# Kernel optimization log

Measured on AMD Instinct MI355X. Metric: run time of the kernel, lower is better.

## Reference

```python
import jax, jax.numpy as jnp
import numpy as np

B, L, IDIM = 1, 1024, 2048
H, DK, DV, K = 16, 128, 128, 4
KEY_DIM = H * DK          # 2048
VAL_DIM = H * DV          # 2048
CONV_DIM = 2 * KEY_DIM + VAL_DIM  # 6144
EPS = 1e-6


def setup_inputs() -> dict:
    key = jax.random.key(0)
    ks = jax.random.split(key, 8)
    s = 0.02
    x = jax.random.normal(ks[0], (B, L, IDIM), jnp.float32)
    Wqkv = jax.random.normal(ks[1], (IDIM, CONV_DIM), jnp.float32) * s
    Wz = jax.random.normal(ks[2], (IDIM, VAL_DIM), jnp.float32) * s
    Wb = jax.random.normal(ks[3], (IDIM, H), jnp.float32) * s
    Wa = jax.random.normal(ks[4], (IDIM, H), jnp.float32) * s
    conv_w = jax.random.normal(ks[5], (CONV_DIM, 1, K), jnp.float32) * 0.2  # depthwise [O,I/g=1,K]
    A_log = jnp.log(jax.random.uniform(ks[6], (H,), jnp.float32, 0.1, 16.0))
    dt_bias = jnp.ones((H,), jnp.float32)
    norm_w = jnp.ones((DV,), jnp.float32)
    Wout = jax.random.normal(ks[7], (VAL_DIM, IDIM), jnp.float32) * s
    return dict(x=x, Wqkv=Wqkv, Wz=Wz, Wb=Wb, Wa=Wa, conv_w=conv_w,
                A_log=A_log, dt_bias=dt_bias, norm_w=norm_w, Wout=Wout)


def _l2norm(t):
    return t * jax.lax.rsqrt(jnp.sum(t * t, axis=-1, keepdims=True) + EPS)


def reference(x, Wqkv, Wz, Wb, Wa, conv_w, A_log, dt_bias, norm_w, Wout):
    b, l, _ = x.shape
    # fused QKV projection + causal depthwise conv + SiLU
    qkv = jnp.einsum('bld,dc->blc', x, Wqkv)                 # [B,L,CONV_DIM]
    qkv = jnp.transpose(qkv, (0, 2, 1))                      # [B,C,L]
    qkv = jax.lax.conv_general_dilated(
        qkv, conv_w, window_strides=(1,), padding=[(K - 1, 0)],
        dimension_numbers=('NCL', 'OIL', 'NCL'), feature_group_count=CONV_DIM)
    qkv = jax.nn.silu(jnp.transpose(qkv, (0, 2, 1)))         # [B,L,C]
    q, k, v = jnp.split(qkv, [KEY_DIM, 2 * KEY_DIM], axis=-1)

    z = jnp.einsum('bld,dv->blv', x, Wz)                     # [B,L,VAL_DIM]
    beta = jax.nn.sigmoid(jnp.einsum('bld,dh->blh', x, Wb))  # [B,L,H]
    A = -jnp.exp(A_log)                                      # [H]
    dt = jax.nn.softplus(jnp.einsum('bld,dh->blh', x, Wa) + dt_bias)
    g = dt * A                                               # [B,L,H] (negative)

    q = _l2norm(q.reshape(b, l, H, DK))
    k = _l2norm(k.reshape(b, l, H, DK))
    v = v.reshape(b, l, H, DV)
    scale = DK ** -0.5

    # time-major for scan: [L,B,H,...]
    qs = jnp.transpose(q, (1, 0, 2, 3)) * scale
    ks_ = jnp.transpose(k, (1, 0, 2, 3))
    vs = jnp.transpose(v, (1, 0, 2, 3))
    bs = jnp.transpose(beta, (1, 0, 2))
    gs = jnp.transpose(g, (1, 0, 2))

    M0 = jnp.zeros((b, H, DK, DV), jnp.float32)

    def step(M, inp):
        q_t, k_t, v_t, b_t, g_t = inp
        M = M * jnp.exp(g_t)[..., None, None]                    # decay
        Mk = jnp.einsum('bhd,bhdv->bhv', k_t, M)                 # readout of old mem
        M = M + jnp.einsum('bhd,bhv->bhdv', k_t, (v_t - Mk) * b_t[..., None])
        o_t = jnp.einsum('bhd,bhdv->bhv', q_t, M)
        return M, o_t

    _, out = jax.lax.scan(step, M0, (qs, ks_, vs, bs, gs))   # out: [L,B,H,DV]
    out = jnp.transpose(out, (1, 0, 2, 3))                   # [B,L,H,DV]

    # RMSNormGated: rms_norm(o) * weight * silu(z)
    zg = z.reshape(b, l, H, DV)
    rms = jax.lax.rsqrt(jnp.mean(out * out, axis=-1, keepdims=True) + EPS)
    out = (out * rms) * norm_w * jax.nn.silu(zg)

    out = out.reshape(b, l, VAL_DIM)
    return jnp.einsum('blv,vd->bld', out, Wout)
```

## Files before the change

### kernel.cpp

```cpp
#include <hip/hip_runtime.h>

typedef short bf16x8 __attribute__((ext_vector_type(8)));
typedef float f32x4 __attribute__((ext_vector_type(4)));
typedef float f32x2 __attribute__((ext_vector_type(2)));
typedef unsigned short u16;
typedef u16 u16x4 __attribute__((ext_vector_type(4)));

#define L_SEQ 1024
#define IDIM_ 2048
#define H_ 16
#define DK_ 128
#define DV_ 128
#define KEYD 2048
#define VALD 2048
#define CONVD 6144
#define QZD 8320
#define GCOL 8192
#define CH 16
#define NCH (L_SEQ / CH)
#define SCH 64
#define NSC (L_SEQ / SCH)

__device__ __forceinline__ u16 f2bf(float f) {
  union { float f; unsigned u; } v; v.f = f;
  unsigned r = v.u + 0x7FFF + ((v.u >> 16) & 1);
  return (u16)(r >> 16);
}

__device__ __forceinline__ float red16(float x) {
  union U { float f; int i; } a, t;
  a.f = x;
  t.i = __builtin_amdgcn_update_dpp(0, a.i, 0xB1, 0xF, 0xF, true); a.f += t.f;
  t.i = __builtin_amdgcn_update_dpp(0, a.i, 0x4E, 0xF, 0xF, true); a.f += t.f;
  t.i = __builtin_amdgcn_update_dpp(0, a.i, 0x141, 0xF, 0xF, true); a.f += t.f;
  t.i = __builtin_amdgcn_update_dpp(0, a.i, 0x140, 0xF, 0xF, true); a.f += t.f;
  return a.f;
}

__device__ __forceinline__ void gl_lds16(const float* g, float* l) {
  __builtin_amdgcn_global_load_lds(
      (const __attribute__((address_space(1))) void*)g,
      (__attribute__((address_space(3))) void*)l, 16, 0, 0);
}
__device__ __forceinline__ void gl_lds4(const float* g, float* l) {
  __builtin_amdgcn_global_load_lds(
      (const __attribute__((address_space(1))) void*)g,
      (__attribute__((address_space(3))) void*)l, 4, 0, 0);
}

__global__ __launch_bounds__(256) void prepcast_kernel(const float* __restrict__ x,
                                                       const float* __restrict__ Wqkv,
                                                       const float* __restrict__ Wz,
                                                       const float* __restrict__ Wb,
                                                       const float* __restrict__ Wa,
                                                       const float* __restrict__ Wout,
                                                       u16* __restrict__ xb,
                                                       u16* __restrict__ WcatT,
                                                       u16* __restrict__ WoutT) {
  __shared__ float tile[32][33];
  const int bid = blockIdx.x;
  if (bid < 2048) {
    int i = (bid * 256 + threadIdx.x) * 4;
    f32x4 v = *(const f32x4*)&x[i];
    u16x4 o = { f2bf(v[0]), f2bf(v[1]), f2bf(v[2]), f2bf(v[3]) };
    *(u16x4*)&xb[i] = o;
    return;
  }
  if (bid >= 22592) {
    size_t off = (size_t)8224 * IDIM_ + (size_t)(bid - 22592) * 8192 + threadIdx.x * 32;
    u16x4 z = {0, 0, 0, 0};
#pragma unroll
    for (int j = 0; j < 8; ++j) *(u16x4*)&WcatT[off + j * 4] = z;
    return;
  }
  if (bid >= 22528) {
    int by = bid - 22528;
    int r = threadIdx.x >> 3, c8 = threadIdx.x & 7;
    int row = by * 32 + r;
#pragma unroll
    for (int cc = 0; cc < 2; ++cc) {
      int c = cc * 8 + c8;
      WcatT[(size_t)(GCOL + c) * IDIM_ + row]      = f2bf(Wb[(size_t)row * 16 + c]);
      WcatT[(size_t)(GCOL + 16 + c) * IDIM_ + row] = f2bf(Wa[(size_t)row * 16 + c]);
    }
    return;
  }
  const float* W; u16* WT; int R, C, bx, by;
  if (bid < 14336) {
    int t = bid - 2048;  bx = t % 192; by = t / 192;
    W = Wqkv; WT = WcatT; R = IDIM_; C = CONVD;
  } else if (bid < 18432) {
    int t = bid - 14336; bx = t & 63; by = t >> 6;
    W = Wz; WT = WcatT + (size_t)CONVD * IDIM_; R = IDIM_; C = VALD;
  } else {
    int t = bid - 18432; bx = t & 63; by = t >> 6;
    W = Wout; WT = WoutT; R = VALD; C = IDIM_;
  }
  int c0 = bx * 32, r0 = by * 32;
  int tx = threadIdx.x & 31, ty = threadIdx.x >> 5;
#pragma unroll
  for (int j = 0; j < 4; ++j)
    tile[ty + j * 8][tx] = W[(size_t)(r0 + ty + j * 8) * C + c0 + tx];
  __syncthreads();
#pragma unroll
  for (int j = 0; j < 4; ++j)
    WT[(size_t)(c0 + ty + j * 8) * R + r0 + tx] = f2bf(tile[tx][ty + j * 8]);
}

__global__ __launch_bounds__(256) void gemm_bt_kernel(const u16* __restrict__ A,
                                                      const u16* __restrict__ B,
                                                      float* __restrict__ C,
                                                      int M, int N, int K) {
  __shared__ short As[128 * 72];
  __shared__ short Bs[128 * 72];
  const int tid = threadIdx.x;
  const int lane = tid & 63, wave = tid >> 6;
  const int wm = wave >> 1, wn = wave & 1;
  const int m0 = blockIdx.y * 128, n0 = blockIdx.x * 128;
  const int l15 = lane & 15, lhi = lane >> 4;

  f32x4 acc[4][4] = {};

  for (int k0 = 0; k0 < K; k0 += 64) {
    __syncthreads();
#pragma unroll
    for (int i = 0; i < 4; ++i) {
      int chunk = tid + i * 256;
      int row = chunk >> 3;
      int kc = (chunk & 7) * 8;
      *(bf16x8*)&As[row * 72 + kc] =
          *(const bf16x8*)&A[(size_t)(m0 + row) * K + k0 + kc];
      *(bf16x8*)&Bs[row * 72 + kc] =
          *(const bf16x8*)&B[(size_t)(n0 + row) * K + k0 + kc];
    }
    __syncthreads();
#pragma unroll
    for (int kk = 0; kk < 64; kk += 32) {
      const int koff = kk + lhi * 8;
      bf16x8 a[4], b[4];
#pragma unroll
      for (int m = 0; m < 4; ++m)
        a[m] = *(const bf16x8*)&As[(wm * 64 + m * 16 + l15) * 72 + koff];
#pragma unroll
      for (int n = 0; n < 4; ++n)
        b[n] = *(const bf16x8*)&Bs[(wn * 64 + n * 16 + l15) * 72 + koff];
#pragma unroll
      for (int m = 0; m < 4; ++m)
#pragma unroll
        for (int n = 0; n < 4; ++n)
          acc[m][n] = __builtin_amdgcn_mfma_f32_16x16x32_bf16(a[m], b[n], acc[m][n], 0, 0, 0);
    }
  }
#pragma unroll
  for (int m = 0; m < 4; ++m)
#pragma unroll
    for (int n = 0; n < 4; ++n)
#pragma unroll
      for (int j = 0; j < 4; ++j) {
        int row = m0 + wm * 64 + m * 16 + lhi * 4 + j;
        int col = n0 + wn * 64 + n * 16 + l15;
        C[(size_t)row * N + col] = acc[m][n][j];
      }
}

__global__ __launch_bounds__(256) void gemm_bt64_kernel(const u16* __restrict__ A,
                                                        const u16* __restrict__ B,
                                                        float* __restrict__ C,
                                                        int M, int N, int K, int cxl) {
  __shared__ short As[64 * 72];
  __shared__ short Bs[128 * 72];
  const int tid = threadIdx.x;
  const int lane = tid & 63, wave = tid >> 6;
  const int wm = wave >> 1, wn = wave & 1;
  const int bid = blockIdx.x;
  const int xcd = bid & 7, bi = bid >> 3;
  const int bx = (xcd << cxl) + (bi & ((1 << cxl) - 1));
  const int by = bi >> cxl;
  const int m0 = by * 64, n0 = bx * 128;
  const int l15 = lane & 15, lhi = lane >> 4;

  f32x4 acc[2][4] = {};

  for (int k0 = 0; k0 < K; k0 += 64) {
    __syncthreads();
#pragma unroll
    for (int i = 0; i < 2; ++i) {
      int chunk = tid + i * 256;
      int row = chunk >> 3;
      int kc = (chunk & 7) * 8;
      *(bf16x8*)&As[row * 72 + kc] =
          *(const bf16x8*)&A[(size_t)(m0 + row) * K + k0 + kc];
    }
#pragma unroll
    for (int i = 0; i < 4; ++i) {
      int chunk = tid + i * 256;
      int row = chunk >> 3;
      int kc = (chunk & 7) * 8;
      *(bf16x8*)&Bs[row * 72 + kc] =
          *(const bf16x8*)&B[(size_t)(n0 + row) * K + k0 + kc];
    }
    __syncthreads();
#pragma unroll
    for (int kk = 0; kk < 64; kk += 32) {
      const int koff = kk + lhi * 8;
      bf16x8 a[2], b[4];
#pragma unroll
      for (int m = 0; m < 2; ++m)
        a[m] = *(const bf16x8*)&As[(wm * 32 + m * 16 + l15) * 72 + koff];
#pragma unroll
      for (int n = 0; n < 4; ++n)
        b[n] = *(const bf16x8*)&Bs[(wn * 64 + n * 16 + l15) * 72 + koff];
#pragma unroll
      for (int m = 0; m < 2; ++m)
#pragma unroll
        for (int n = 0; n < 4; ++n)
          acc[m][n] = __builtin_amdgcn_mfma_f32_16x16x32_bf16(a[m], b[n], acc[m][n], 0, 0, 0);
    }
  }
#pragma unroll
  for (int m = 0; m < 2; ++m)
#pragma unroll
    for (int n = 0; n < 4; ++n)
#pragma unroll
      for (int j = 0; j < 4; ++j) {
        int row = m0 + wm * 32 + m * 16 + lhi * 4 + j;
        int col = n0 + wn * 64 + n * 16 + l15;
        C[(size_t)row * N + col] = acc[m][n][j];
      }
}

__global__ __launch_bounds__(256) void gatelite_kernel(const float* __restrict__ qkvz,
                                                       const float* __restrict__ A_log,
                                                       const float* __restrict__ dt_bias,
                                                       float* __restrict__ btT,
                                                       float* __restrict__ egT,
                                                       float* __restrict__ gT) {
  int gid = blockIdx.x * 256 + threadIdx.x;
  int l = gid >> 4, h = gid & 15;
  const float* row = qkvz + (size_t)l * QZD + GCOL;
  float b = row[h], a = row[16 + h];
  btT[h * L_SEQ + l] = 1.f / (1.f + expf(-b));
  float dtv = a + dt_bias[h];
  dtv = (dtv > 20.f) ? dtv : log1pf(expf(dtv));
  float g = -expf(A_log[h]) * dtv;
  egT[h * L_SEQ + l] = expf(g);
  gT[h * L_SEQ + l] = g;
}

__global__ __launch_bounds__(256) void prep2_kernel(const float* __restrict__ qkvz,
                                                    const float* __restrict__ cw,
                                                    float* __restrict__ qn,
                                                    float* __restrict__ kn,
                                                    float* __restrict__ vT) {
  __shared__ float tile[32][33];
  const int bid = blockIdx.x;
  if (bid < 4096) {
    int wid = bid * 4 + (threadIdx.x >> 6);
    int lane = threadIdx.x & 63;
    int l = wid >> 4, h = wid & 15;
    const int cq = h * 128 + lane * 2;
    const int ck = KEYD + cq;
    const float* row0 = qkvz + (size_t)l * QZD;
    f32x4 wq0 = *(const f32x4*)&cw[cq * 4];
    f32x4 wq1 = *(const f32x4*)&cw[(cq + 1) * 4];
    f32x4 wk0 = *(const f32x4*)&cw[ck * 4];
    f32x4 wk1 = *(const f32x4*)&cw[(ck + 1) * 4];
    f32x2 xq = *(const f32x2*)&row0[cq];
    f32x2 xk = *(const f32x2*)&row0[ck];
    float q0 = xq[0] * wq0[3], q1 = xq[1] * wq1[3];
    float k0 = xk[0] * wk0[3], k1 = xk[1] * wk1[3];
    if (l >= 1) {
      f32x2 aq = *(const f32x2*)&row0[cq - QZD];
      f32x2 ak = *(const f32x2*)&row0[ck - QZD];
      q0 += aq[0] * wq0[2]; q1 += aq[1] * wq1[2];
      k0 += ak[0] * wk0[2]; k1 += ak[1] * wk1[2];
    }
    if (l >= 2) {
      f32x2 aq = *(const f32x2*)&row0[cq - 2 * QZD];
      f32x2 ak = *(const f32x2*)&row0[ck - 2 * QZD];
      q0 += aq[0] * wq0[1]; q1 += aq[1] * wq1[1];
      k0 += ak[0] * wk0[1]; k1 += ak[1] * wk1[1];
    }
    if (l >= 3) {
      f32x2 aq = *(const f32x2*)&row0[cq - 3 * QZD];
      f32x2 ak = *(const f32x2*)&row0[ck - 3 * QZD];
      q0 += aq[0] * wq0[0]; q1 += aq[1] * wq1[0];
      k0 += ak[0] * wk0[0]; k1 += ak[1] * wk1[0];
    }
    f32x2 qv = { q0 / (1.f + expf(-q0)), q1 / (1.f + expf(-q1)) };
    f32x2 kv = { k0 / (1.f + expf(-k0)), k1 / (1.f + expf(-k1)) };

    float ssq = qv[0] * qv[0] + qv[1] * qv[1];
    float ssk = kv[0] * kv[0] + kv[1] * kv[1];
#pragma unroll
    for (int s = 1; s < 64; s <<= 1) {
      ssq += __shfl_xor(ssq, s);
      ssk += __shfl_xor(ssk, s);
    }
    float scq = 0.08838834764831845f / sqrtf(ssq + 1e-6f);
    float sck = 1.f / sqrtf(ssk + 1e-6f);
    qv[0] *= scq; qv[1] *= scq;
    kv[0] *= sck; kv[1] *= sck;
    size_t base = ((size_t)h * L_SEQ + l) * 128 + lane * 2;
    *(f32x2*)&qn[base] = qv;
    *(f32x2*)&kn[base] = kv;
    return;
  }
  int t = bid - 4096;
  int c0 = (t & 63) * 32, l0 = (t >> 6) * 32;
  int tx = threadIdx.x & 31, ty = threadIdx.x >> 5;
  const int c = 2 * KEYD + c0 + tx;
  f32x4 w = *(const f32x4*)&cw[c * 4];
#pragma unroll
  for (int j = 0; j < 4; ++j) {
    int l = l0 + ty + j * 8;
    const float* p = qkvz + (size_t)l * QZD + c;
    float s = p[0] * w[3];
    if (l >= 1) s += p[-QZD] * w[2];
    if (l >= 2) s += p[-2 * QZD] * w[1];
    if (l >= 3) s += p[-3 * QZD] * w[0];
    tile[ty + j * 8][tx] = s / (1.f + expf(-s));
  }
  __syncthreads();
#pragma unroll
  for (int j = 0; j < 4; ++j)
    vT[(size_t)(c0 + ty + j * 8) * L_SEQ + l0 + tx] = tile[tx][ty + j * 8];
}

__global__ __launch_bounds__(256) void scan_kernel(const float* __restrict__ kn,
                                                   const float* __restrict__ vT,
                                                   const float* __restrict__ egT,
                                                   const float* __restrict__ btT,
                                                   float* __restrict__ Mb,
                                                   float* __restrict__ DbT) {
  __shared__ alignas(16) float ks[2][CH][128];
  __shared__ alignas(16) float vs[2][16][CH];
  __shared__ alignas(16) float ebc[2][2][CH];

  const int tid = threadIdx.x;
  const int wave = tid >> 6, lane = tid & 63;
  const int dk_sub = lane & 15;
  const int head = blockIdx.x & 15;
  const int dv0 = (blockIdx.x >> 4) * 16;
  const int col_local = tid >> 4;
  const int dv = dv0 + col_local;

  const float* kh = kn + (size_t)head * L_SEQ * 128;

  auto stage = [&](int chunk, int buf) {
    const int l0 = chunk * CH;
    const float* kg = kh + (size_t)l0 * 128;
#pragma unroll
    for (int i = 0; i < 2; ++i) {
      int seg = i * 4 + wave;
      int off = seg * 256 + lane * 4;
      gl_lds16(kg + off, &ks[buf][0][0] + seg * 256);
    }
    {
      int idx = wave * 64 + lane;
      gl_lds4(vT + (size_t)(head * 128 + dv0 + (idx >> 4)) * L_SEQ + l0 + (idx & 15),
              &vs[buf][0][0] + wave * 64);
    }
    if (wave == 0 && lane < 32) {
      const float* src = (lane < 16) ? (egT + head * L_SEQ + l0 + lane)
                                     : (btT + head * L_SEQ + l0 + (lane - 16));
      gl_lds4(src, &ebc[buf][0][0]);
    }
  };

  stage(0, 0);
  __syncthreads();

  f32x4 Mlo = {0.f, 0.f, 0.f, 0.f}, Mhi = {0.f, 0.f, 0.f, 0.f};
  const int dkb = dk_sub * 8;
  float* dcol = DbT + (size_t)(head * 128 + dv) * L_SEQ;

#pragma unroll 1
  for (int c = 0; c < NCH; ++c) {
    const int buf = c & 1;
    if (c + 1 < NCH) stage(c + 1, buf ^ 1);

    if ((c & 3) == 0) {
      int sc = c >> 2;
      float* mrow = Mb + (((size_t)sc * 16 + head) * 128 + dv) * 128 + dkb;
      *(f32x4*)mrow = Mlo;
      *(f32x4*)(mrow + 4) = Mhi;
    }

    f32x4 ev[4], bv[4], vv[4];
#pragma unroll
    for (int i = 0; i < 4; ++i) {
      ev[i] = *(const f32x4*)&ebc[buf][0][i * 4];
      bv[i] = *(const f32x4*)&ebc[buf][1][i * 4];
      vv[i] = *(const f32x4*)&vs[buf][col_local][i * 4];
    }
    f32x4 kr[4][2];
#pragma unroll
    for (int i = 0; i < 3; ++i) {
      kr[i][0] = *(const f32x4*)&ks[buf][i][dkb];
      kr[i][1] = *(const f32x4*)&ks[buf][i][dkb + 4];
    }

#pragma unroll
    for (int s = 0; s < CH; ++s) {
      if (s + 3 < CH) {
        kr[(s + 3) & 3][0] = *(const f32x4*)&ks[buf][s + 3][dkb];
        kr[(s + 3) & 3][1] = *(const f32x4*)&ks[buf][s + 3][dkb + 4];
      }
      const f32x4 k0 = kr[s & 3][0], k1 = kr[s & 3][1];
      const float e = ev[s >> 2][s & 3], b = bv[s >> 2][s & 3];
      const float v = vv[s >> 2][s & 3];

      float skm0 = k0[0] * Mlo[0], skm1 = k0[1] * Mlo[1];
      skm0 = fmaf(k0[2], Mlo[2], skm0); skm1 = fmaf(k0[3], Mlo[3], skm1);
      skm0 = fmaf(k1[0], Mhi[0], skm0); skm1 = fmaf(k1[1], Mhi[1], skm1);
      skm0 = fmaf(k1[2], Mhi[2], skm0); skm1 = fmaf(k1[3], Mhi[3], skm1);
      f32x4 emlo, emhi;
#pragma unroll
      for (int i = 0; i < 4; ++i) { emlo[i] = e * Mlo[i]; emhi[i] = e * Mhi[i]; }
      float skm = red16(skm0 + skm1);
      float dl = (v - e * skm) * b;
      if (dk_sub == 0) dcol[c * CH + s] = dl;
#pragma unroll
      for (int i = 0; i < 4; ++i) {
        Mlo[i] = fmaf(k0[i], dl, emlo[i]);
        Mhi[i] = fmaf(k1[i], dl, emhi[i]);
      }
    }
    __syncthreads();
  }
}

__global__ __launch_bounds__(256) void opass_kernel(const float* __restrict__ qn,
                                                    const float* __restrict__ kn,
                                                    const float* __restrict__ DbT,
                                                    const float* __restrict__ gT,
                                                    const float* __restrict__ Mb,
                                                    const float* __restrict__ qkvz,
                                                    const float* __restrict__ norm_w,
                                                    u16* __restrict__ gn) {
  __shared__ alignas(16) u16 qsb[64][136];
  __shared__ alignas(16) u16 bbuf[128][136];
  __shared__ alignas(16) u16 Asb[64][72];
  __shared__ float gsh[64], Gh[64];
  __shared__ float ssr[2][64];

  const int tid = threadIdx.x;
  const int lane = tid & 63, wave = tid >> 6;
  const int l15 = lane & 15, lhi = lane >> 4;
  const int h = blockIdx.x & 15, sc = blockIdx.x >> 4;
  const int l0 = sc * SCH;

  {
    int t = tid >> 2, c0 = (tid & 3) * 32;
    const float* qr = qn + ((size_t)h * L_SEQ + l0 + t) * 128 + c0;
    const float* kr = kn + ((size_t)h * L_SEQ + l0 + t) * 128 + c0;
#pragma unroll
    for (int j = 0; j < 8; ++j) {
      f32x4 vq = *(const f32x4*)&qr[j * 4];
      f32x4 vk = *(const f32x4*)&kr[j * 4];
      u16x4 oq = { f2bf(vq[0]), f2bf(vq[1]), f2bf(vq[2]), f2bf(vq[3]) };
      u16x4 ok = { f2bf(vk[0]), f2bf(vk[1]), f2bf(vk[2]), f2bf(vk[3]) };
      *(u16x4*)&qsb[t][c0 + j * 4] = oq;
      *(u16x4*)&bbuf[t][c0 + j * 4] = ok;
    }
  }
  if (tid < 64) gsh[tid] = gT[h * L_SEQ + l0 + tid];
  __syncthreads();
  if (tid < 64) {
    float a = 0.f;
    for (int u = 0; u <= tid; ++u) a += gsh[u];
    Gh[tid] = a;
  }
  __syncthreads();

  f32x4 acc1[2][2] = {};
  const int wm = wave >> 1, wn = wave & 1;
#pragma unroll
  for (int kk = 0; kk < 128; kk += 32) {
    const int koff = kk + lhi * 8;
    bf16x8 a[2], b[2];
#pragma unroll
    for (int m = 0; m < 2; ++m)
      a[m] = *(const bf16x8*)&qsb[wm * 32 + m * 16 + l15][koff];
#pragma unroll
    for (int n = 0; n < 2; ++n)
      b[n] = *(const bf16x8*)&bbuf[wn * 32 + n * 16 + l15][koff];
#pragma unroll
    for (int m = 0; m < 2; ++m)
#pragma unroll
      for (int n = 0; n < 2; ++n)
        acc1[m][n] = __builtin_amdgcn_mfma_f32_16x16x32_bf16(a[m], b[n], acc1[m][n], 0, 0, 0);
  }
#pragma unroll
  for (int m = 0; m < 2; ++m)
#pragma unroll
    for (int n = 0; n < 2; ++n)
#pragma unroll
      for (int j = 0; j < 4; ++j) {
        int t = wm * 32 + m * 16 + lhi * 4 + j;
        int s = wn * 32 + n * 16 + l15;
        float a = (s <= t) ? acc1[m][n][j] * expf(Gh[t] - Gh[s]) : 0.f;
        Asb[t][s] = f2bf(a);
      }
  __syncthreads();

  {
    int dv = tid >> 1, c0 = (tid & 1) * 64;
    const float* mr = Mb + (((size_t)sc * 16 + h) * 128 + dv) * 128 + c0;
#pragma unroll
    for (int j = 0; j < 16; ++j) {
      f32x4 v = *(const f32x4*)&mr[j * 4];
      u16x4 o = { f2bf(v[0]), f2bf(v[1]), f2bf(v[2]), f2bf(v[3]) };
      *(u16x4*)&bbuf[dv][c0 + j * 4] = o;
    }
  }
  __syncthreads();

  f32x4 acc[2][4] = {};
#pragma unroll
  for (int kk = 0; kk < 128; kk += 32) {
    const int koff = kk + lhi * 8;
    bf16x8 a[2], b[4];
#pragma unroll
    for (int m = 0; m < 2; ++m)
      a[m] = *(const bf16x8*)&qsb[wm * 32 + m * 16 + l15][koff];
#pragma unroll
    for (int n = 0; n < 4; ++n)
      b[n] = *(const bf16x8*)&bbuf[wn * 64 + n * 16 + l15][koff];
#pragma unroll
    for (int m = 0; m < 2; ++m)
#pragma unroll
      for (int n = 0; n < 4; ++n)
        acc[m][n] = __builtin_amdgcn_mfma_f32_16x16x32_bf16(a[m], b[n], acc[m][n], 0, 0, 0);
  }
#pragma unroll
  for (int m = 0; m < 2; ++m) {
#pragma unroll
    for (int j = 0; j < 4; ++j) {
      int t = wm * 32 + m * 16 + lhi * 4 + j;
      float sc1 = expf(Gh[t]);
#pragma unroll
      for (int n = 0; n < 4; ++n) acc[m][n][j] *= sc1;
    }
  }
  __syncthreads();

  {
    int dv = tid >> 1, c0 = (tid & 1) * 32;
    const float* dr = DbT + (size_t)(h * 128 + dv) * L_SEQ + l0 + c0;
#pragma unroll
    for (int j = 0; j < 8; ++j) {
      f32x4 v = *(const f32x4*)&dr[j * 4];
      u16x4 o = { f2bf(v[0]), f2bf(v[1]), f2bf(v[2]), f2bf(v[3]) };
      *(u16x4*)&bbuf[dv][c0 + j * 4] = o;
    }
  }
  __syncthreads();

#pragma unroll
  for (int kk = 0; kk < 64; kk += 32) {
    const int koff = kk + lhi * 8;
    bf16x8 a[2], b[4];
#pragma unroll
    for (int m = 0; m < 2; ++m)
      a[m] = *(const bf16x8*)&Asb[wm * 32 + m * 16 + l15][koff];
#pragma unroll
    for (int n = 0; n < 4; ++n)
      b[n] = *(const bf16x8*)&bbuf[wn * 64 + n * 16 + l15][koff];
#pragma unroll
    for (int m = 0; m < 2; ++m)
#pragma unroll
      for (int n = 0; n < 4; ++n)
        acc[m][n] = __builtin_amdgcn_mfma_f32_16x16x32_bf16(a[m], b[n], acc[m][n], 0, 0, 0);
  }

  float pr[2][4];
#pragma unroll
  for (int m = 0; m < 2; ++m)
#pragma unroll
    for (int j = 0; j < 4; ++j) {
      float p = 0.f;
#pragma unroll
      for (int n = 0; n < 4; ++n) p = fmaf(acc[m][n][j], acc[m][n][j], p);
      pr[m][j] = red16(p);
    }
  if (l15 == 0) {
#pragma unroll
    for (int m = 0; m < 2; ++m)
#pragma unroll
      for (int j = 0; j < 4; ++j)
        ssr[wn][wm * 32 + m * 16 + lhi * 4 + j] = pr[m][j];
  }
  __syncthreads();
#pragma unroll
  for (int m = 0; m < 2; ++m)
#pragma unroll
    for (int j = 0; j < 4; ++j) {
      int t = wm * 32 + m * 16 + lhi * 4 + j;
      float ss = ssr[0][t] + ssr[1][t];
      float r = 1.f / sqrtf(ss * (1.f / 128.f) + 1e-6f);
      const float* zp = qkvz + (size_t)(l0 + t) * QZD + CONVD + h * 128;
      u16* dst = gn + (size_t)(l0 + t) * VALD + h * 128;
#pragma unroll
      for (int n = 0; n < 4; ++n) {
        int dv = wn * 64 + n * 16 + l15;
        float z = zp[dv];
        float sil = z / (1.f + expf(-z));
        dst[dv] = f2bf(acc[m][n][j] * r * norm_w[dv] * sil);
      }
    }
}

extern "C" void kernel_launch(void* const* d_in, const int* in_sizes, int n_in,
                              void* d_out, int out_size, void* d_ws, size_t ws_size,
                              hipStream_t stream) {
  const float* x      = (const float*)d_in[0];
  const float* Wqkv   = (const float*)d_in[1];
  const float* Wz     = (const float*)d_in[2];
  const float* Wb     = (const float*)d_in[3];
  const float* Wa     = (const float*)d_in[4];
  const float* conv_w = (const float*)d_in[5];
  const float* A_log  = (const float*)d_in[6];
  const float* dt_bias= (const float*)d_in[7];
  const float* norm_w = (const float*)d_in[8];
  const float* Wout   = (const float*)d_in[9];
  float* out = (float*)d_out;

  char* ws = (char*)d_ws;
  size_t off = 0;
  auto alloc = [&](size_t bytes) {
    void* p = ws + off;
    off = (off + bytes + 255) & ~(size_t)255;
    return p;
  };
  u16* xb     = (u16*)alloc((size_t)L_SEQ * IDIM_ * 2);
  u16* WcatT  = (u16*)alloc((size_t)QZD * IDIM_ * 2);
  u16* WoutT  = (u16*)alloc((size_t)IDIM_ * VALD * 2);
  float* qkvz = (float*)alloc((size_t)L_SEQ * QZD * 4);
  float* qn   = (float*)alloc((size_t)H_ * L_SEQ * 128 * 4);
  float* kn   = (float*)alloc((size_t)H_ * L_SEQ * 128 * 4);
  float* vT   = (float*)alloc((size_t)H_ * 128 * L_SEQ * 4);
  float* btT  = (float*)alloc((size_t)L_SEQ * H_ * 4);
  float* egT  = (float*)alloc((size_t)L_SEQ * H_ * 4);
  float* gTb  = (float*)alloc((size_t)L_SEQ * H_ * 4);
  float* Mb   = (float*)alloc((size_t)NSC * H_ * 128 * 128 * 4);
  float* DbT  = (float*)alloc((size_t)H_ * 128 * L_SEQ * 4);
  u16* gn     = (u16*)alloc((size_t)L_SEQ * VALD * 2);

  prepcast_kernel<<<22616, 256, 0, stream>>>(x, Wqkv, Wz, Wb, Wa, Wout, xb, WcatT, WoutT);

  gemm_bt_kernel<<<dim3(QZD / 128, L_SEQ / 128), 256, 0, stream>>>(xb, WcatT, qkvz, L_SEQ, QZD, IDIM_);

  gatelite_kernel<<<64, 256, 0, stream>>>(qkvz, A_log, dt_bias, btT, egT, gTb);

  prep2_kernel<<<6144, 256, 0, stream>>>(qkvz, conv_w, qn, kn, vT);

  scan_kernel<<<H_ * (DV_ / 16), 256, 0, stream>>>(kn, vT, egT, btT, Mb, DbT);

  opass_kernel<<<NSC * H_, 256, 0, stream>>>(qn, kn, DbT, gTb, Mb, qkvz, norm_w, gn);

  gemm_bt64_kernel<<<256, 256, 0, stream>>>(gn, WoutT, out, L_SEQ, IDIM_, VALD, 1);
}
```

Before: 322.0 us.

## Replace sequential delta-rule scan with chunked WY-form inversion and chunk-level state updates

Replaces the per-timestep recurrent scan (16-step chunks, DPP reductions per step) with a chunked WY formulation. A new kernel builds the intra-chunk k·k^T matrix with bf16 MFMA and forward-substitutes to get the 64x64 inverse per chunk and head. A second kernel then advances the state once per 64-step chunk using matrix products instead of per-step updates. This removes the serial per-timestep dependency chain. In exchange it adds an extra kernel and workspace traffic, bf16 rounding in the k·k^T term, and scalar LDS loops run by a single wave for the triangular solve.

Measured after the change: 363.2 us. +12.8%, slower.

```diff
diff --git a/kernel.cpp b/kernel.cpp
--- a/kernel.cpp
+++ b/kernel.cpp
@@ -16,8 +16,6 @@
 #define CONVD 6144
 #define QZD 8320
 #define GCOL 8192
-#define CH 16
-#define NCH (L_SEQ / CH)
 #define SCH 64
 #define NSC (L_SEQ / SCH)
 
@@ -35,17 +33,6 @@
   t.i = __builtin_amdgcn_update_dpp(0, a.i, 0x141, 0xF, 0xF, true); a.f += t.f;
   t.i = __builtin_amdgcn_update_dpp(0, a.i, 0x140, 0xF, 0xF, true); a.f += t.f;
   return a.f;
-}
-
-__device__ __forceinline__ void gl_lds16(const float* g, float* l) {
-  __builtin_amdgcn_global_load_lds(
-      (const __attribute__((address_space(1))) void*)g,
-      (__attribute__((address_space(3))) void*)l, 16, 0, 0);
-}
-__device__ __forceinline__ void gl_lds4(const float* g, float* l) {
-  __builtin_amdgcn_global_load_lds(
-      (const __attribute__((address_space(1))) void*)g,
-      (__attribute__((address_space(3))) void*)l, 4, 0, 0);
 }
 
 __global__ __launch_bounds__(256) void prepcast_kernel(const float* __restrict__ x,
@@ -233,7 +220,6 @@
                                                        const float* __restrict__ A_log,
                                                        const float* __restrict__ dt_bias,
                                                        float* __restrict__ btT,
-                                                       float* __restrict__ egT,
                                                        float* __restrict__ gT) {
   int gid = blockIdx.x * 256 + threadIdx.x;
   int l = gid >> 4, h = gid & 15;
@@ -242,9 +228,7 @@
   btT[h * L_SEQ + l] = 1.f / (1.f + expf(-b));
   float dtv = a + dt_bias[h];
   dtv = (dtv > 20.f) ? dtv : log1pf(expf(dtv));
-  float g = -expf(A_log[h]) * dtv;
-  egT[h * L_SEQ + l] = expf(g);
-  gT[h * L_SEQ + l] = g;
+  gT[h * L_SEQ + l] = -expf(A_log[h]) * dtv;
 }
 
 __global__ __launch_bounds__(256) void prep2_kernel(const float* __restrict__ qkvz,
@@ -327,104 +311,191 @@
     vT[(size_t)(c0 + ty + j * 8) * L_SEQ + l0 + tx] = tile[tx][ty + j * 8];
 }
 
-__global__ __launch_bounds__(256) void scan_kernel(const float* __restrict__ kn,
-                                                   const float* __restrict__ vT,
-                                                   const float* __restrict__ egT,
+__global__ __launch_bounds__(256) void winv_kernel(const float* __restrict__ kn,
+                                                   const float* __restrict__ gT,
                                                    const float* __restrict__ btT,
-                                                   float* __restrict__ Mb,
-                                                   float* __restrict__ DbT) {
-  __shared__ alignas(16) float ks[2][CH][128];
-  __shared__ alignas(16) float vs[2][16][CH];
-  __shared__ alignas(16) float ebc[2][2][CH];
+                                                   float* __restrict__ Wg) {
+  __shared__ alignas(16) u16 kb[64][136];
+  __shared__ float Nl[64][65];
+  __shared__ float gsh[64], Gh[64], bts[64];
 
   const int tid = threadIdx.x;
-  const int wave = tid >> 6, lane = tid & 63;
-  const int dk_sub = lane & 15;
-  const int head = blockIdx.x & 15;
-  const int dv0 = (blockIdx.x >> 4) * 16;
-  const int col_local = tid >> 4;
-  const int dv = dv0 + col_local;
-
-  const float* kh = kn + (size_t)head * L_SEQ * 128;
-
-  auto stage = [&](int chunk, int buf) {
-    const int l0 = chunk * CH;
-    const float* kg = kh + (size_t)l0 * 128;
-#pragma unroll
-    for (int i = 0; i < 2; ++i) {
-      int seg = i * 4 + wave;
-      int off = seg * 256 + lane * 4;
-      gl_lds16(kg + off, &ks[buf][0][0] + seg * 256);
-    }
+  const int lane = tid & 63, wave = tid >> 6;
+  const int l15 = lane & 15, lhi = lane >> 4;
+  const int h = blockIdx.x & 15, sc = blockIdx.x >> 4;
+  const int l0 = sc * SCH;
+
+  {
+    int t = tid >> 2, c0 = (tid & 3) * 32;
+    const float* kr = kn + ((size_t)h * L_SEQ + l0 + t) * 128 + c0;
+#pragma unroll
+    for (int j = 0; j < 8; ++j) {
+      f32x4 vk = *(const f32x4*)&kr[j * 4];
+      u16x4 ok = { f2bf(vk[0]), f2bf(vk[1]), f2bf(vk[2]), f2bf(vk[3]) };
+      *(u16x4*)&kb[t][c0 + j * 4] = ok;
+    }
+  }
+  if (tid < 64) {
+    gsh[tid] = gT[h * L_SEQ + l0 + tid];
+    bts[tid] = btT[h * L_SEQ + l0 + tid];
+  }
+  __syncthreads();
+  if (tid < 64) {
+    float a = 0.f;
+    for (int u = 0; u <= tid; ++u) a += gsh[u];
+    Gh[tid] = a;
+  }
+  __syncthreads();
+
+  f32x4 acc1[2][2] = {};
+  const int wm = wave >> 1, wn = wave & 1;
+#pragma unroll
+  for (int kk = 0; kk < 128; kk += 32) {
+    const int koff = kk + lhi * 8;
+    bf16x8 a[2], b[2];
+#pragma unroll
+    for (int m = 0; m < 2; ++m)
+      a[m] = *(const bf16x8*)&kb[wm * 32 + m * 16 + l15][koff];
+#pragma unroll
+    for (int n = 0; n < 2; ++n)
+      b[n] = *(const bf16x8*)&kb[wn * 32 + n * 16 + l15][koff];
+#pragma unroll
+    for (int m = 0; m < 2; ++m)
+#pragma unroll
+      for (int n = 0; n < 2; ++n)
+        acc1[m][n] = __builtin_amdgcn_mfma_f32_16x16x32_bf16(a[m], b[n], acc1[m][n], 0, 0, 0);
+  }
+#pragma unroll
+  for (int m = 0; m < 2; ++m)
+#pragma unroll
+    for (int n = 0; n < 2; ++n)
+#pragma unroll
+      for (int j = 0; j < 4; ++j) {
+        int t = wm * 32 + m * 16 + lhi * 4 + j;
+        int s = wn * 32 + n * 16 + l15;
+        Nl[t][s] = (s < t) ? bts[t] * expf(Gh[t] - Gh[s]) * acc1[m][n][j] : 0.f;
+      }
+  __syncthreads();
+
+  if (wave == 0) {
+    float w[64];
+    w[0] = (lane == 0) ? 1.f : 0.f;
+#pragma unroll
+    for (int t = 1; t < 64; ++t) {
+      float a0 = (lane == t) ? 1.f : 0.f, a1 = 0.f;
+#pragma unroll
+      for (int s = 0; s + 1 < t; s += 2) {
+        a0 = fmaf(-Nl[t][s], w[s], a0);
+        a1 = fmaf(-Nl[t][s + 1], w[s + 1], a1);
+      }
+      if (t & 1) a0 = fmaf(-Nl[t][t - 1], w[t - 1], a0);
+      w[t] = a0 + a1;
+    }
+    size_t base = (size_t)(sc * 16 + h) * 4096 + (size_t)lane * 64;
+#pragma unroll
+    for (int s = 0; s < 64; ++s) Wg[base + s] = w[s];
+  }
+}
+
+__global__ __launch_bounds__(256) void wyscan_kernel(const float* __restrict__ kn,
+                                                     const float* __restrict__ vT,
+                                                     const float* __restrict__ gT,
+                                                     const float* __restrict__ btT,
+                                                     const float* __restrict__ Wg,
+                                                     float* __restrict__ Mb,
+                                                     float* __restrict__ DbT) {
+  __shared__ float klds[128][65];
+  __shared__ float Mlds[128][9];
+  __shared__ float WldsT[64][65];
+  __shared__ float rlds[64][9];
+  __shared__ float dlds[64][9];
+  __shared__ float gsh[64], Gh[64], bts[64];
+
+  const int tid = threadIdx.x;
+  const int lane = tid & 63, wave = tid >> 6;
+  const int h = blockIdx.x & 15, dvb = blockIdx.x >> 4;
+  const int dv0 = dvb * 8;
+  const int dva = wave * 2, dvb2 = wave * 2 + 1;
+
+  for (int i = tid; i < 128 * 9; i += 256) Mlds[i / 9][i % 9] = 0.f;
+  __syncthreads();
+
+#pragma unroll 1
+  for (int c = 0; c < NSC; ++c) {
+    const int l0 = c * SCH;
     {
-      int idx = wave * 64 + lane;
-      gl_lds4(vT + (size_t)(head * 128 + dv0 + (idx >> 4)) * L_SEQ + l0 + (idx & 15),
-              &vs[buf][0][0] + wave * 64);
-    }
-    if (wave == 0 && lane < 32) {
-      const float* src = (lane < 16) ? (egT + head * L_SEQ + l0 + lane)
-                                     : (btT + head * L_SEQ + l0 + (lane - 16));
-      gl_lds4(src, &ebc[buf][0][0]);
-    }
-  };
-
-  stage(0, 0);
-  __syncthreads();
-
-  f32x4 Mlo = {0.f, 0.f, 0.f, 0.f}, Mhi = {0.f, 0.f, 0.f, 0.f};
-  const int dkb = dk_sub * 8;
-  float* dcol = DbT + (size_t)(head * 128 + dv) * L_SEQ;
-
-#pragma unroll 1
-  for (int c = 0; c < NCH; ++c) {
-    const int buf = c & 1;
-    if (c + 1 < NCH) stage(c + 1, buf ^ 1);
-
-    if ((c & 3) == 0) {
-      int sc = c >> 2;
-      float* mrow = Mb + (((size_t)sc * 16 + head) * 128 + dv) * 128 + dkb;
-      *(f32x4*)mrow = Mlo;
-      *(f32x4*)(mrow + 4) = Mhi;
-    }
-
-    f32x4 ev[4], bv[4], vv[4];
-#pragma unroll
-    for (int i = 0; i < 4; ++i) {
-      ev[i] = *(const f32x4*)&ebc[buf][0][i * 4];
-      bv[i] = *(const f32x4*)&ebc[buf][1][i * 4];
-      vv[i] = *(const f32x4*)&vs[buf][col_local][i * 4];
-    }
-    f32x4 kr[4][2];
-#pragma unroll
-    for (int i = 0; i < 3; ++i) {
-      kr[i][0] = *(const f32x4*)&ks[buf][i][dkb];
-      kr[i][1] = *(const f32x4*)&ks[buf][i][dkb + 4];
-    }
-
-#pragma unroll
-    for (int s = 0; s < CH; ++s) {
-      if (s + 3 < CH) {
-        kr[(s + 3) & 3][0] = *(const f32x4*)&ks[buf][s + 3][dkb];
-        kr[(s + 3) & 3][1] = *(const f32x4*)&ks[buf][s + 3][dkb + 4];
-      }
-      const f32x4 k0 = kr[s & 3][0], k1 = kr[s & 3][1];
-      const float e = ev[s >> 2][s & 3], b = bv[s >> 2][s & 3];
-      const float v = vv[s >> 2][s & 3];
-
-      float skm0 = k0[0] * Mlo[0], skm1 = k0[1] * Mlo[1];
-      skm0 = fmaf(k0[2], Mlo[2], skm0); skm1 = fmaf(k0[3], Mlo[3], skm1);
-      skm0 = fmaf(k1[0], Mhi[0], skm0); skm1 = fmaf(k1[1], Mhi[1], skm1);
-      skm0 = fmaf(k1[2], Mhi[2], skm0); skm1 = fmaf(k1[3], Mhi[3], skm1);
-      f32x4 emlo, emhi;
-#pragma unroll
-      for (int i = 0; i < 4; ++i) { emlo[i] = e * Mlo[i]; emhi[i] = e * Mhi[i]; }
-      float skm = red16(skm0 + skm1);
-      float dl = (v - e * skm) * b;
-      if (dk_sub == 0) dcol[c * CH + s] = dl;
-#pragma unroll
-      for (int i = 0; i < 4; ++i) {
-        Mlo[i] = fmaf(k0[i], dl, emlo[i]);
-        Mhi[i] = fmaf(k1[i], dl, emhi[i]);
+      int t = tid >> 2, c0 = (tid & 3) * 32;
+      const float* kr = kn + ((size_t)h * L_SEQ + l0 + t) * 128 + c0;
+#pragma unroll
+      for (int j = 0; j < 32; ++j) klds[c0 + j][t] = kr[j];
+    }
+    {
+      size_t base = (size_t)(c * 16 + h) * 4096;
+      for (int i = tid; i < 4096; i += 256) WldsT[i >> 6][i & 63] = Wg[base + i];
+    }
+    if (tid < 64) {
+      gsh[tid] = gT[h * L_SEQ + l0 + tid];
+      bts[tid] = btT[h * L_SEQ + l0 + tid];
+    }
+    {
+      int dv = tid >> 5, dk0 = (tid & 31) * 4;
+      float* mr = Mb + (((size_t)(c * 16 + h)) * 128 + dv0 + dv) * 128 + dk0;
+#pragma unroll
+      for (int j = 0; j < 4; ++j) mr[j] = Mlds[dk0 + j][dv];
+    }
+    __syncthreads();
+    if (tid == 0) {
+      float a = 0.f;
+      for (int u = 0; u < 64; ++u) { a += gsh[u]; Gh[u] = a; }
+    }
+    __syncthreads();
+
+    {
+      const int t = lane;
+      float a0 = 0.f, a1 = 0.f;
+      for (int dk = 0; dk < 128; ++dk) {
+        float kv = klds[dk][t];
+        a0 = fmaf(kv, Mlds[dk][dva], a0);
+        a1 = fmaf(kv, Mlds[dk][dvb2], a1);
+      }
+      float egt = expf(Gh[t]);
+      float bt = bts[t];
+      float v0 = vT[(size_t)(h * 128 + dv0 + dva) * L_SEQ + l0 + t];
+      float v1 = vT[(size_t)(h * 128 + dv0 + dvb2) * L_SEQ + l0 + t];
+      rlds[t][dva]  = bt * (v0 - egt * a0);
+      rlds[t][dvb2] = bt * (v1 - egt * a1);
+    }
+    __syncthreads();
+
+    {
+      const int t = lane;
+      float a0 = 0.f, a1 = 0.f;
+      for (int s = 0; s < 64; ++s) {
+        float wv = WldsT[s][t];
+        a0 = fmaf(wv, rlds[s][dva], a0);
+        a1 = fmaf(wv, rlds[s][dvb2], a1);
+      }
+      DbT[(size_t)(h * 128 + dv0 + dva) * L_SEQ + l0 + t]  = a0;
+      DbT[(size_t)(h * 128 + dv0 + dvb2) * L_SEQ + l0 + t] = a1;
+      float e63t = expf(Gh[63] - Gh[t]);
+      dlds[t][dva]  = a0 * e63t;
+      dlds[t][dvb2] = a1 * e63t;
+    }
+    __syncthreads();
+
+    {
+      const float E63 = expf(Gh[63]);
+#pragma unroll
+      for (int rep = 0; rep < 2; ++rep) {
+        const int dk = lane + rep * 64;
+#pragma unroll
+        for (int dvi = 0; dvi < 2; ++dvi) {
+          const int dv = wave * 2 + dvi;
+          float acc = E63 * Mlds[dk][dv];
+          for (int s = 0; s < 64; ++s)
+            acc = fmaf(klds[dk][s], dlds[s][dv], acc);
+          Mlds[dk][dv] = acc;
+        }
       }
     }
     __syncthreads();
@@ -642,8 +713,8 @@
   float* kn   = (float*)alloc((size_t)H_ * L_SEQ * 128 * 4);
   float* vT   = (float*)alloc((size_t)H_ * 128 * L_SEQ * 4);
   float* btT  = (float*)alloc((size_t)L_SEQ * H_ * 4);
-  float* egT  = (float*)alloc((size_t)L_SEQ * H_ * 4);
   float* gTb  = (float*)alloc((size_t)L_SEQ * H_ * 4);
+  float* Wgb  = (float*)alloc((size_t)NSC * H_ * 64 * 64 * 4);
   float* Mb   = (float*)alloc((size_t)NSC * H_ * 128 * 128 * 4);
   float* DbT  = (float*)alloc((size_t)H_ * 128 * L_SEQ * 4);
   u16* gn     = (u16*)alloc((size_t)L_SEQ * VALD * 2);
@@ -652,11 +723,12 @@
 
   gemm_bt_kernel<<<dim3(QZD / 128, L_SEQ / 128), 256, 0, stream>>>(xb, WcatT, qkvz, L_SEQ, QZD, IDIM_);
 
-  gatelite_kernel<<<64, 256, 0, stream>>>(qkvz, A_log, dt_bias, btT, egT, gTb);
+  gatelite_kernel<<<64, 256, 0, stream>>>(qkvz, A_log, dt_bias, btT, gTb);
 
   prep2_kernel<<<6144, 256, 0, stream>>>(qkvz, conv_w, qn, kn, vT);
 
-  scan_kernel<<<H_ * (DV_ / 16), 256, 0, stream>>>(kn, vT, egT, btT, Mb, DbT);
+  winv_kernel<<<NSC * H_, 256, 0, stream>>>(kn, gTb, btT, Wgb);
+  wyscan_kernel<<<256, 256, 0, stream>>>(kn, vT, gTb, btT, Wgb, Mb, DbT);
 
   opass_kernel<<<NSC * H_, 256, 0, stream>>>(qn, kn, DbT, gTb, Mb, qkvz, norm_w, gn);
 
```
